# Kernel tuning notes

Measured on AMD Instinct MI355X. Metric: run time of the kernel, lower is better.

Reference implementation:

```python
import jax, jax.numpy as jnp
import numpy as np

N = 50000        # nodes
E = 800000       # edges
D = 128          # input_dim
H = 128          # hidden_dim
G = 256          # graphs in batch


def setup_inputs() -> dict:
    key = jax.random.key(0)
    ks = jax.random.split(key, 9)
    x = jax.random.normal(ks[0], (N, D), dtype=jnp.float32)
    edge_index = jax.random.randint(ks[1], (2, E), 0, N, dtype=jnp.int32)
    batch = jnp.sort(jax.random.randint(ks[2], (N,), 0, G, dtype=jnp.int32))
    s0 = 1.0 / np.sqrt(D)
    s1 = 1.0 / np.sqrt(H)
    W0 = jax.random.uniform(ks[3], (D, H), jnp.float32, -s0, s0)
    b0 = jnp.zeros((H,), jnp.float32)
    alpha0 = jnp.full((H,), 0.25, jnp.float32)   # PReLU init
    W1 = jax.random.uniform(ks[4], (H, H), jnp.float32, -s1, s1)
    b1 = jnp.zeros((H,), jnp.float32)
    alpha1 = jnp.full((H,), 0.25, jnp.float32)
    return {"x": x, "edge_index": edge_index, "batch": batch,
            "W0": W0, "b0": b0, "alpha0": alpha0,
            "W1": W1, "b1": b1, "alpha1": alpha1}


def _prelu(z, alpha):
    return jnp.where(z > 0, z, alpha * z)


def reference(x, edge_index, batch, W0, b0, alpha0, W1, b1, alpha1):
    # Add self-loops (PyG GCNConv default)
    loops = jnp.arange(N, dtype=edge_index.dtype)
    src = jnp.concatenate([edge_index[0], loops])   # [E+N]
    dst = jnp.concatenate([edge_index[1], loops])   # [E+N]

    # Symmetric degree normalization: deg computed on destination (with self-loops)
    deg = jax.ops.segment_sum(jnp.ones_like(src, dtype=x.dtype), dst, num_segments=N)
    dinv = jax.lax.rsqrt(deg)                        # deg >= 1 due to self-loops
    norm = dinv[src] * dinv[dst]                     # [E+N]

    def gcn_conv(z, W, b):
        zw = z @ W                                   # [N,H] small GEMM
        msg = zw[src] * norm[:, None]                # [E+N,H] gather+scale
        return jax.ops.segment_sum(msg, dst, num_segments=N) + b

    z1 = _prelu(gcn_conv(x, W0, b0), alpha0)         # [N,H]
    z2 = _prelu(gcn_conv(z1, W1, b1), alpha1)        # [N,H]

    # global_add_pool per layer, then concat along features -> [G, 2H]
    g = jnp.concatenate([
        jax.ops.segment_sum(z1, batch, num_segments=G),
        jax.ops.segment_sum(z2, batch, num_segments=G),
    ], axis=1)
    return z2, g
```

## Files before the change

kernel.cpp:

```cpp
#include <hip/hip_runtime.h>

#define TPB 256
#define PROWS 32

typedef unsigned int uint32;
typedef unsigned short ushort16;

typedef __attribute__((ext_vector_type(8))) short bf16x8;
typedef __attribute__((ext_vector_type(4))) float f32x4;

__device__ __forceinline__ unsigned short f2bf(float f) {
  union { float f; unsigned int i; } c; c.f = f;
  unsigned int r = c.i + 0x7fffu + ((c.i >> 16) & 1u);
  return (unsigned short)(r >> 16);
}

__device__ __forceinline__ float bflo(uint32 p) {
  union { unsigned int i; float f; } c; c.i = p << 16; return c.f;
}
__device__ __forceinline__ float bfhi(uint32 p) {
  union { unsigned int i; float f; } c; c.i = p & 0xffff0000u; return c.f;
}

__device__ __forceinline__ float bf16val(ushort16 u) {
  union { unsigned int i; float f; } c; c.i = ((uint32)u) << 16; return c.f;
}

__global__ void prep_kernel(int* __restrict__ deg, int N,
                            int* __restrict__ g, int ng,
                            const float* __restrict__ W0, ushort16* __restrict__ wt0,
                            const float* __restrict__ W1, ushort16* __restrict__ wt1) {
  int i = blockIdx.x * blockDim.x + threadIdx.x;
  int stride = gridDim.x * blockDim.x;
  for (int j = i; j < N; j += stride) deg[j] = 0;
  for (int j = i; j < ng; j += stride) g[j] = 0;
  for (int j = i; j < 16384; j += stride) {
    int k = j >> 7, c = j & 127;
    wt0[(size_t)c * 128 + k] = f2bf(W0[j]);
    wt1[(size_t)c * 128 + k] = f2bf(W1[j]);
  }
}

__global__ void count_rank_kernel(const int* __restrict__ dst, int E,
                                  int* __restrict__ deg,
                                  unsigned short* __restrict__ rank) {
  int i = blockIdx.x * blockDim.x + threadIdx.x;
  if (i < E) rank[i] = (unsigned short)atomicAdd(&deg[dst[i]], 1);
}

__global__ void scan_block_kernel(const int* __restrict__ in, int n,
                                  int* __restrict__ out_excl, int* __restrict__ bsum,
                                  float* __restrict__ dinv) {
  __shared__ int sh[TPB];
  int t = threadIdx.x;
  int i = blockIdx.x * TPB + t;
  int v = (i < n) ? in[i] : 0;
  if (dinv != nullptr && i < n) dinv[i] = 1.0f / sqrtf((float)(v + 1));
  sh[t] = v;
  __syncthreads();
  for (int off = 1; off < TPB; off <<= 1) {
    int x = (t >= off) ? sh[t - off] : 0;
    __syncthreads();
    sh[t] += x;
    __syncthreads();
  }
  if (i < n) out_excl[i] = sh[t] - v;
  if (t == TPB - 1 && bsum != nullptr) bsum[blockIdx.x] = sh[t];
}

__global__ void scan_fixup_kernel(int* __restrict__ rs, const int* __restrict__ boff,
                                  int n, int total) {
  int i = blockIdx.x * TPB + threadIdx.x;
  if (i < n) rs[i] += boff[blockIdx.x];
  else if (i == n) rs[n] = total;
}

__global__ __launch_bounds__(256) void fill_gemm0_kernel(
    const float* __restrict__ A, const ushort16* __restrict__ wt,
    const float* __restrict__ dinv, ushort16* __restrict__ outz, int nrows,
    int gemmBlocks,
    const int* __restrict__ src, const int* __restrict__ dst,
    const unsigned short* __restrict__ rank, const int* __restrict__ rs,
    int E, unsigned short* __restrict__ col) {
  __shared__ ushort16 Abf[64][128];
  int t = threadIdx.x;

  if (blockIdx.x >= gemmBlocks) {
    int i = (blockIdx.x - gemmBlocks) * TPB + t;
    if (i < E) {
      int d = dst[i];
      col[rs[d] + (int)rank[i]] = (unsigned short)src[i];
    }
    return;
  }

  int r0 = blockIdx.x * 64;
  {
    const float4* __restrict__ A4 = (const float4*)A;
#pragma unroll
    for (int i = 0; i < 8; ++i) {
      int idx = t + 256 * i;
      int r = idx >> 5;
      int cc = idx & 31;
      float4 v = make_float4(0.f, 0.f, 0.f, 0.f);
      if (r0 + r < nrows) v = A4[(size_t)(r0 + r) * 32 + cc];
      ushort4 p;
      p.x = f2bf(v.x); p.y = f2bf(v.y); p.z = f2bf(v.z); p.w = f2bf(v.w);
      *(ushort4*)&Abf[r][cc * 4] = p;
    }
  }
  __syncthreads();

  int wave = t >> 6;
  int lane = t & 63;
  int lrow = lane & 15;
  int kg = lane >> 4;
  int rBase = wave * 16;

  f32x4 acc[8];
#pragma unroll
  for (int ct = 0; ct < 8; ++ct) acc[ct] = (f32x4){0.f, 0.f, 0.f, 0.f};

#pragma unroll
  for (int ks = 0; ks < 4; ++ks) {
    bf16x8 af = *(const bf16x8*)&Abf[rBase + lrow][ks * 32 + kg * 8];
#pragma unroll
    for (int ct = 0; ct < 8; ++ct) {
      bf16x8 bfr = *(const bf16x8*)&wt[(size_t)(ct * 16 + lrow) * 128 + ks * 32 + kg * 8];
      acc[ct] = __builtin_amdgcn_mfma_f32_16x16x32_bf16(af, bfr, acc[ct], 0, 0, 0);
    }
  }

  __syncthreads();

#pragma unroll
  for (int reg = 0; reg < 4; ++reg) {
    int rl = rBase + kg * 4 + reg;
    int grow = r0 + rl;
    float di = (grow < nrows) ? dinv[grow] : 0.f;
#pragma unroll
    for (int ct = 0; ct < 8; ++ct) {
      Abf[rl][ct * 16 + lrow] = f2bf(di * acc[ct][reg]);
    }
  }
  __syncthreads();

  {
#pragma unroll
    for (int i = 0; i < 4; ++i) {
      int idx = t + 256 * i;
      int r = idx >> 4;
      int cc = idx & 15;
      if (r0 + r < nrows)
        ((uint4*)&outz[(size_t)(r0 + r) * 128])[cc] = ((const uint4*)&Abf[r][0])[cc];
    }
  }
}

__global__ __launch_bounds__(256) void gemm_mfma_bf16_kernel(
    const ushort16* __restrict__ Ain, const ushort16* __restrict__ wt,
    const float* __restrict__ dinv, ushort16* __restrict__ out, int nrows) {
  __shared__ ushort16 Abf[64][128];
  int t = threadIdx.x;
  int r0 = blockIdx.x * 64;

  {
    const uint4* __restrict__ A16 = (const uint4*)Ain;
#pragma unroll
    for (int i = 0; i < 4; ++i) {
      int idx = t + 256 * i;
      int r = idx >> 4;
      int cc = idx & 15;
      uint4 v = make_uint4(0u, 0u, 0u, 0u);
      if (r0 + r < nrows) v = A16[(size_t)(r0 + r) * 16 + cc];
      *(uint4*)&Abf[r][cc * 8] = v;
    }
  }
  __syncthreads();

  int wave = t >> 6;
  int lane = t & 63;
  int lrow = lane & 15;
  int kg = lane >> 4;
  int rBase = wave * 16;

  f32x4 acc[8];
#pragma unroll
  for (int ct = 0; ct < 8; ++ct) acc[ct] = (f32x4){0.f, 0.f, 0.f, 0.f};

#pragma unroll
  for (int ks = 0; ks < 4; ++ks) {
    bf16x8 af = *(const bf16x8*)&Abf[rBase + lrow][ks * 32 + kg * 8];
#pragma unroll
    for (int ct = 0; ct < 8; ++ct) {
      bf16x8 bfr = *(const bf16x8*)&wt[(size_t)(ct * 16 + lrow) * 128 + ks * 32 + kg * 8];
      acc[ct] = __builtin_amdgcn_mfma_f32_16x16x32_bf16(af, bfr, acc[ct], 0, 0, 0);
    }
  }

  __syncthreads();

#pragma unroll
  for (int reg = 0; reg < 4; ++reg) {
    int rl = rBase + kg * 4 + reg;
    int grow = r0 + rl;
    float di = (grow < nrows) ? dinv[grow] : 0.f;
#pragma unroll
    for (int ct = 0; ct < 8; ++ct) {
      Abf[rl][ct * 16 + lrow] = f2bf(di * acc[ct][reg]);
    }
  }
  __syncthreads();

  {
#pragma unroll
    for (int i = 0; i < 4; ++i) {
      int idx = t + 256 * i;
      int r = idx >> 4;
      int cc = idx & 15;
      if (r0 + r < nrows)
        ((uint4*)&out[(size_t)(r0 + r) * 128])[cc] = ((const uint4*)&Abf[r][0])[cc];
    }
  }
}

__global__ __launch_bounds__(256) void aggregate_kernel(
    const ushort16* __restrict__ zws, const int* __restrict__ rs,
    const unsigned short* __restrict__ col,
    const float* __restrict__ dinv, const float* __restrict__ bias,
    const float* __restrict__ alpha,
    float* __restrict__ outf, ushort16* __restrict__ outh, int nrows) {
  int wid = threadIdx.x >> 6;
  int lane = threadIdx.x & 63;
  int node = blockIdx.x * 4 + wid;
  if (node >= nrows) return;
  int c = lane * 2;

  uint32 pv = *(const uint32*)&zws[(size_t)node * 128 + c];
  float accx = bflo(pv), accy = bfhi(pv);

  int e0 = rs[node], e1 = rs[node + 1];
  for (int base = e0; base < e1; base += 64) {
    int nb = e1 - base; if (nb > 64) nb = 64;
    int colv = (base + lane < e1) ? (int)col[base + lane] : 0;
    int j = 0;
    for (; j + 8 <= nb; j += 8) {
      int s0 = __shfl(colv, j + 0);
      int s1 = __shfl(colv, j + 1);
      int s2 = __shfl(colv, j + 2);
      int s3 = __shfl(colv, j + 3);
      int s4 = __shfl(colv, j + 4);
      int s5 = __shfl(colv, j + 5);
      int s6 = __shfl(colv, j + 6);
      int s7 = __shfl(colv, j + 7);
      uint32 p0 = *(const uint32*)&zws[(size_t)s0 * 128 + c];
      uint32 p1 = *(const uint32*)&zws[(size_t)s1 * 128 + c];
      uint32 p2 = *(const uint32*)&zws[(size_t)s2 * 128 + c];
      uint32 p3 = *(const uint32*)&zws[(size_t)s3 * 128 + c];
      uint32 p4 = *(const uint32*)&zws[(size_t)s4 * 128 + c];
      uint32 p5 = *(const uint32*)&zws[(size_t)s5 * 128 + c];
      uint32 p6 = *(const uint32*)&zws[(size_t)s6 * 128 + c];
      uint32 p7 = *(const uint32*)&zws[(size_t)s7 * 128 + c];
      accx += bflo(p0) + bflo(p1) + bflo(p2) + bflo(p3)
            + bflo(p4) + bflo(p5) + bflo(p6) + bflo(p7);
      accy += bfhi(p0) + bfhi(p1) + bfhi(p2) + bfhi(p3)
            + bfhi(p4) + bfhi(p5) + bfhi(p6) + bfhi(p7);
    }
    if (j < nb) {
      int last = nb - 1;
      int i0 = j + 0, i1 = j + 1, i2 = j + 2, i3 = j + 3;
      int i4 = j + 4, i5 = j + 5, i6 = j + 6, i7 = j + 7;
      int s0 = __shfl(colv, i0 < last ? i0 : last);
      int s1 = __shfl(colv, i1 < last ? i1 : last);
      int s2 = __shfl(colv, i2 < last ? i2 : last);
      int s3 = __shfl(colv, i3 < last ? i3 : last);
      int s4 = __shfl(colv, i4 < last ? i4 : last);
      int s5 = __shfl(colv, i5 < last ? i5 : last);
      int s6 = __shfl(colv, i6 < last ? i6 : last);
      int s7 = __shfl(colv, i7 < last ? i7 : last);
      float m0 = (i0 < nb) ? 1.f : 0.f, m1 = (i1 < nb) ? 1.f : 0.f;
      float m2 = (i2 < nb) ? 1.f : 0.f, m3 = (i3 < nb) ? 1.f : 0.f;
      float m4 = (i4 < nb) ? 1.f : 0.f, m5 = (i5 < nb) ? 1.f : 0.f;
      float m6 = (i6 < nb) ? 1.f : 0.f, m7 = (i7 < nb) ? 1.f : 0.f;
      uint32 p0 = *(const uint32*)&zws[(size_t)s0 * 128 + c];
      uint32 p1 = *(const uint32*)&zws[(size_t)s1 * 128 + c];
      uint32 p2 = *(const uint32*)&zws[(size_t)s2 * 128 + c];
      uint32 p3 = *(const uint32*)&zws[(size_t)s3 * 128 + c];
      uint32 p4 = *(const uint32*)&zws[(size_t)s4 * 128 + c];
      uint32 p5 = *(const uint32*)&zws[(size_t)s5 * 128 + c];
      uint32 p6 = *(const uint32*)&zws[(size_t)s6 * 128 + c];
      uint32 p7 = *(const uint32*)&zws[(size_t)s7 * 128 + c];
      accx += m0 * bflo(p0) + m1 * bflo(p1) + m2 * bflo(p2) + m3 * bflo(p3)
            + m4 * bflo(p4) + m5 * bflo(p5) + m6 * bflo(p6) + m7 * bflo(p7);
      accy += m0 * bfhi(p0) + m1 * bfhi(p1) + m2 * bfhi(p2) + m3 * bfhi(p3)
            + m4 * bfhi(p4) + m5 * bfhi(p5) + m6 * bfhi(p6) + m7 * bfhi(p7);
    }
  }

  float di = dinv[node];
  float2 b = *(const float2*)&bias[c];
  float2 al = *(const float2*)&alpha[c];
  float zx = di * accx + b.x, zy = di * accy + b.y;
  zx = zx > 0.f ? zx : al.x * zx;
  zy = zy > 0.f ? zy : al.y * zy;
  if (outh != nullptr) {
    uint32 packed = (uint32)f2bf(zx) | ((uint32)f2bf(zy) << 16);
    *(uint32*)&outh[(size_t)node * 128 + c] = packed;
  } else {
    float2 r; r.x = zx; r.y = zy;
    *(float2*)&outf[(size_t)node * 128 + c] = r;
  }
}

__global__ __launch_bounds__(256) void pool_kernel(const ushort16* __restrict__ z1h,
                                                   const float* __restrict__ z2,
                                                   const int* __restrict__ batch, int n,
                                                   float* __restrict__ g) {
  int r0 = blockIdx.x * PROWS;
  int t = threadIdx.x;
  __shared__ int bsh[PROWS];
  int rmax = n - r0; if (rmax > PROWS) rmax = PROWS;
  if (t < PROWS && t < rmax) bsh[t] = batch[r0 + t];
  __syncthreads();

  int c = t & 127;
  float acc = 0.f;
  int cur = bsh[0];
  if (t < 128) {
    for (int i = 0; i < rmax; ++i) {
      int b = bsh[i];
      if (b != cur) {
        atomicAdd(&g[(size_t)cur * 256 + t], acc);
        acc = 0.f;
        cur = b;
      }
      acc += bf16val(z1h[(size_t)(r0 + i) * 128 + c]);
    }
  } else {
    for (int i = 0; i < rmax; ++i) {
      int b = bsh[i];
      if (b != cur) {
        atomicAdd(&g[(size_t)cur * 256 + t], acc);
        acc = 0.f;
        cur = b;
      }
      acc += z2[(size_t)(r0 + i) * 128 + c];
    }
  }
  atomicAdd(&g[(size_t)cur * 256 + t], acc);
}

extern "C" void kernel_launch(void* const* d_in, const int* in_sizes, int n_in,
                              void* d_out, int out_size, void* d_ws, size_t ws_size,
                              hipStream_t stream) {
  const float* x     = (const float*)d_in[0];
  const int*   ei    = (const int*)d_in[1];
  const int*   batch = (const int*)d_in[2];
  const float* W0    = (const float*)d_in[3];
  const float* b0    = (const float*)d_in[4];
  const float* a0    = (const float*)d_in[5];
  const float* W1    = (const float*)d_in[6];
  const float* b1    = (const float*)d_in[7];
  const float* a1    = (const float*)d_in[8];
  float* out = (float*)d_out;

  const int N = in_sizes[0] / 128;
  const int E = in_sizes[1] / 2;
  const int G = (out_size - N * 128) / 256;

  const int* src  = ei;
  const int* dstp = ei + E;

  int* w = (int*)d_ws;
  size_t o = 0;
  int*            deg    = w + o; o += (size_t)N;
  int*            rs     = w + o; o += (size_t)((N + 1 + 3) & ~3);
  int*            bsum   = w + o; o += 256;
  int*            boff   = w + o; o += 256;
  unsigned short* col    = (unsigned short*)(w + o); o += (size_t)((E + 1) / 2);
  unsigned short* rank   = (unsigned short*)(w + o); o += (size_t)((E + 1) / 2);
  float*          dinv   = (float*)(w + o); o += (size_t)N;
  ushort16*       wt0    = (ushort16*)(w + o); o += 8192;
  ushort16*       wt1    = (ushort16*)(w + o); o += 8192;
  ushort16*       zws    = (ushort16*)(w + o); o += (size_t)N * 64;
  ushort16*       z1h    = (ushort16*)(w + o); o += (size_t)N * 64;
  (void)ws_size; (void)n_in;

  const int blkE = (E + TPB - 1) / TPB;
  const int blkN = (N + TPB - 1) / TPB;
  const int gemmBlocks = (N + 63) / 64;

  float* g = out + (size_t)N * 128;

  prep_kernel<<<512, TPB, 0, stream>>>(deg, N, (int*)g, G * 256, W0, wt0, W1, wt1);

  count_rank_kernel<<<blkE, TPB, 0, stream>>>(dstp, E, deg, rank);

  scan_block_kernel<<<blkN, TPB, 0, stream>>>(deg, N, rs, bsum, dinv);
  scan_block_kernel<<<1, TPB, 0, stream>>>(bsum, blkN, boff, nullptr, nullptr);
  scan_fixup_kernel<<<(N + TPB) / TPB, TPB, 0, stream>>>(rs, boff, N, E);

  fill_gemm0_kernel<<<gemmBlocks + blkE, TPB, 0, stream>>>(
      x, wt0, dinv, zws, N, gemmBlocks,
      src, dstp, rank, rs, E, col);

  aggregate_kernel<<<(N + 3) / 4, 256, 0, stream>>>(zws, rs, col, dinv, b0, a0,
                                                    nullptr, z1h, N);

  gemm_mfma_bf16_kernel<<<gemmBlocks, 256, 0, stream>>>(z1h, wt1, dinv, zws, N);
  aggregate_kernel<<<(N + 3) / 4, 256, 0, stream>>>(zws, rs, col, dinv, b1, a1,
                                                    out, nullptr, N);

  pool_kernel<<<(N + PROWS - 1) / PROWS, 256, 0, stream>>>(z1h, out, batch, N, g);
}
```

Measured before the change: 189.4 us.

## Merge weight transpose into count kernel and overlap z1 pooling with GEMM1

The bf16 weight transpose moves out of the zeroing kernel into extra blocks appended to the degree-count/rank kernel. The z1 pooling moves into extra blocks of the layer-1 GEMM launch so it runs alongside the GEMM, leaving a z2-only pool kernel at the end. The aim is to shorten the tail and use idle GPU capacity during the small kernels, at the cost of more launch-level heterogeneity. The final pool now covers half the data with 64-row blocks split across two thread halves.

```diff
diff --git a/kernel.cpp b/kernel.cpp
--- a/kernel.cpp
+++ b/kernel.cpp
@@ -1,7 +1,6 @@
 #include <hip/hip_runtime.h>
 
 #define TPB 256
-#define PROWS 32
 
 typedef unsigned int uint32;
 typedef unsigned short ushort16;
@@ -26,26 +25,29 @@
   union { unsigned int i; float f; } c; c.i = ((uint32)u) << 16; return c.f;
 }
 
-__global__ void prep_kernel(int* __restrict__ deg, int N,
-                            int* __restrict__ g, int ng,
-                            const float* __restrict__ W0, ushort16* __restrict__ wt0,
-                            const float* __restrict__ W1, ushort16* __restrict__ wt1) {
+__global__ void zero_kernel(int* __restrict__ deg, int N,
+                            int* __restrict__ g, int ng) {
   int i = blockIdx.x * blockDim.x + threadIdx.x;
   int stride = gridDim.x * blockDim.x;
   for (int j = i; j < N; j += stride) deg[j] = 0;
   for (int j = i; j < ng; j += stride) g[j] = 0;
-  for (int j = i; j < 16384; j += stride) {
-    int k = j >> 7, c = j & 127;
-    wt0[(size_t)c * 128 + k] = f2bf(W0[j]);
-    wt1[(size_t)c * 128 + k] = f2bf(W1[j]);
-  }
-}
-
-__global__ void count_rank_kernel(const int* __restrict__ dst, int E,
-                                  int* __restrict__ deg,
-                                  unsigned short* __restrict__ rank) {
-  int i = blockIdx.x * blockDim.x + threadIdx.x;
-  if (i < E) rank[i] = (unsigned short)atomicAdd(&deg[dst[i]], 1);
+}
+
+__global__ void crwt_kernel(const int* __restrict__ dst, int E,
+                            int* __restrict__ deg, unsigned short* __restrict__ rank,
+                            int crBlocks,
+                            const float* __restrict__ W0, ushort16* __restrict__ wt0,
+                            const float* __restrict__ W1, ushort16* __restrict__ wt1) {
+  int t = threadIdx.x;
+  if (blockIdx.x < crBlocks) {
+    int i = blockIdx.x * TPB + t;
+    if (i < E) rank[i] = (unsigned short)atomicAdd(&deg[dst[i]], 1);
+  } else {
+    int idx = (blockIdx.x - crBlocks) * TPB + t;
+    int k = idx >> 7, c = idx & 127;
+    wt0[(size_t)c * 128 + k] = f2bf(W0[idx]);
+    wt1[(size_t)c * 128 + k] = f2bf(W1[idx]);
+  }
 }
 
 __global__ void scan_block_kernel(const int* __restrict__ in, int n,
@@ -157,13 +159,41 @@
   }
 }
 
-__global__ __launch_bounds__(256) void gemm_mfma_bf16_kernel(
+__global__ __launch_bounds__(256) void gemm1_poolz1_kernel(
     const ushort16* __restrict__ Ain, const ushort16* __restrict__ wt,
-    const float* __restrict__ dinv, ushort16* __restrict__ out, int nrows) {
+    const float* __restrict__ dinv, ushort16* __restrict__ out, int nrows,
+    int gemmBlocks,
+    const int* __restrict__ batch, float* __restrict__ g) {
   __shared__ ushort16 Abf[64][128];
+  __shared__ int bsh[64];
   int t = threadIdx.x;
+
+  if (blockIdx.x >= gemmBlocks) {
+    int r0 = (blockIdx.x - gemmBlocks) * 64;
+    int rmax = nrows - r0; if (rmax > 64) rmax = 64;
+    if (t < 64 && t < rmax) bsh[t] = batch[r0 + t];
+    __syncthreads();
+    int c = t & 127;
+    int lo = (t >> 7) * 32;
+    int hi = lo + 32; if (hi > rmax) hi = rmax;
+    if (lo < rmax) {
+      float acc = 0.f;
+      int cur = bsh[lo];
+      for (int i = lo; i < hi; ++i) {
+        int b = bsh[i];
+        if (b != cur) {
+          atomicAdd(&g[(size_t)cur * 256 + c], acc);
+          acc = 0.f;
+          cur = b;
+        }
+        acc += bf16val(Ain[(size_t)(r0 + i) * 128 + c]);
+      }
+      atomicAdd(&g[(size_t)cur * 256 + c], acc);
+    }
+    return;
+  }
+
   int r0 = blockIdx.x * 64;
-
   {
     const uint4* __restrict__ A16 = (const uint4*)Ain;
 #pragma unroll
@@ -312,42 +342,32 @@
   }
 }
 
-__global__ __launch_bounds__(256) void pool_kernel(const ushort16* __restrict__ z1h,
-                                                   const float* __restrict__ z2,
-                                                   const int* __restrict__ batch, int n,
-                                                   float* __restrict__ g) {
-  int r0 = blockIdx.x * PROWS;
+__global__ __launch_bounds__(256) void pool_z2_kernel(const float* __restrict__ z2,
+                                                      const int* __restrict__ batch,
+                                                      int n, float* __restrict__ g) {
+  __shared__ int bsh[64];
   int t = threadIdx.x;
-  __shared__ int bsh[PROWS];
-  int rmax = n - r0; if (rmax > PROWS) rmax = PROWS;
-  if (t < PROWS && t < rmax) bsh[t] = batch[r0 + t];
-  __syncthreads();
-
+  int r0 = blockIdx.x * 64;
+  int rmax = n - r0; if (rmax > 64) rmax = 64;
+  if (t < 64 && t < rmax) bsh[t] = batch[r0 + t];
+  __syncthreads();
   int c = t & 127;
-  float acc = 0.f;
-  int cur = bsh[0];
-  if (t < 128) {
-    for (int i = 0; i < rmax; ++i) {
+  int lo = (t >> 7) * 32;
+  int hi = lo + 32; if (hi > rmax) hi = rmax;
+  if (lo < rmax) {
+    float acc = 0.f;
+    int cur = bsh[lo];
+    for (int i = lo; i < hi; ++i) {
       int b = bsh[i];
       if (b != cur) {
-        atomicAdd(&g[(size_t)cur * 256 + t], acc);
-        acc = 0.f;
-        cur = b;
-      }
-      acc += bf16val(z1h[(size_t)(r0 + i) * 128 + c]);
-    }
-  } else {
-    for (int i = 0; i < rmax; ++i) {
-      int b = bsh[i];
-      if (b != cur) {
-        atomicAdd(&g[(size_t)cur * 256 + t], acc);
+        atomicAdd(&g[(size_t)cur * 256 + 128 + c], acc);
         acc = 0.f;
         cur = b;
       }
       acc += z2[(size_t)(r0 + i) * 128 + c];
     }
-  }
-  atomicAdd(&g[(size_t)cur * 256 + t], acc);
+    atomicAdd(&g[(size_t)cur * 256 + 128 + c], acc);
+  }
 }
 
 extern "C" void kernel_launch(void* const* d_in, const int* in_sizes, int n_in,
@@ -389,12 +409,14 @@
   const int blkE = (E + TPB - 1) / TPB;
   const int blkN = (N + TPB - 1) / TPB;
   const int gemmBlocks = (N + 63) / 64;
+  const int poolBlocks = (N + 63) / 64;
 
   float* g = out + (size_t)N * 128;
 
-  prep_kernel<<<512, TPB, 0, stream>>>(deg, N, (int*)g, G * 256, W0, wt0, W1, wt1);
-
-  count_rank_kernel<<<blkE, TPB, 0, stream>>>(dstp, E, deg, rank);
+  zero_kernel<<<512, TPB, 0, stream>>>(deg, N, (int*)g, G * 256);
+
+  crwt_kernel<<<blkE + 64, TPB, 0, stream>>>(dstp, E, deg, rank, blkE,
+                                             W0, wt0, W1, wt1);
 
   scan_block_kernel<<<blkN, TPB, 0, stream>>>(deg, N, rs, bsum, dinv);
   scan_block_kernel<<<1, TPB, 0, stream>>>(bsum, blkN, boff, nullptr, nullptr);
@@ -407,9 +429,11 @@
   aggregate_kernel<<<(N + 3) / 4, 256, 0, stream>>>(zws, rs, col, dinv, b0, a0,
                                                     nullptr, z1h, N);
 
-  gemm_mfma_bf16_kernel<<<gemmBlocks, 256, 0, stream>>>(z1h, wt1, dinv, zws, N);
+  gemm1_poolz1_kernel<<<gemmBlocks + poolBlocks, 256, 0, stream>>>(
+      z1h, wt1, dinv, zws, N, gemmBlocks, batch, g);
+
   aggregate_kernel<<<(N + 3) / 4, 256, 0, stream>>>(zws, rs, col, dinv, b1, a1,
                                                     out, nullptr, N);
 
-  pool_kernel<<<(N + PROWS - 1) / PROWS, 256, 0, stream>>>(z1h, out, batch, N, g);
-}
+  pool_z2_kernel<<<poolBlocks, 256, 0, stream>>>(out, batch, N, g);
+}
```

Result: no change. 193.1 us (+2.0%).
